# Kernel tuning notes

Hardware: AMD Instinct MI355X
Metric: run time of the kernel (lower is better)

The kernel has to match this reference:

```python
import jax, jax.numpy as jnp
import numpy as np

P_SIZE = 128   # proto_size
HID = 768      # hidden_size
BATCH = 32
NREL = 16
RATIO = 0.5    # proto_emb_ratio


def setup_inputs() -> dict:
    key = jax.random.key(0)
    k1, k2, k3, k4 = jax.random.split(key, 4)
    return {
        "instance_embedding": jax.random.normal(k1, (BATCH, HID), jnp.float32),
        # small scale keeps sigmoid(p_h @ M_r @ p_t) away from hard saturation
        "relation_embedding": jax.random.normal(k2, (NREL, HID, HID), jnp.float32) * 0.02,
        "rel_label_ids": jax.random.randint(k3, (BATCH, NREL, P_SIZE), 0, P_SIZE + 1, dtype=jnp.int32),
        "labels": jnp.arange(BATCH, dtype=jnp.int32),  # distinct -> torch.unique is exact with static shapes
        "prototypes": jax.random.normal(k4, (P_SIZE, HID), jnp.float32),  # nn.Embedding weight
    }


def reference(instance_embedding, relation_embedding, rel_label_ids, labels, prototypes):
    P, H = prototypes.shape
    B, R, _ = rel_label_ids.shape

    # torch.unique(labels, return_inverse=True): sorted uniques + inverse map.
    labels_unique = jnp.sort(labels)                      # [K] (K == B, labels distinct)
    inv = jnp.argsort(jnp.argsort(labels))                # index_list (rank of each label)
    # original code: index = index_list[k] -> rel rows permuted by inverse map
    rel_k = rel_label_ids[inv]                            # [K,R,P]

    total_nonzero = jnp.sum(rel_label_ids) > 0
    batch_mask = (jnp.sum(rel_k, axis=(1, 2)) > 0)[:, None, None]   # skip if sum(rel[index])==0
    row_mask = (jnp.sum(rel_k, axis=2) > 0)[:, :, None]             # skip if sum(rel[index][i])==0
    m = (rel_k != P) & batch_mask & row_mask & total_nonzero        # [K,R,P] active entries
    mf = m.astype(prototypes.dtype)

    P0 = prototypes                                       # get_proto_embedding(): never updated inside loop
    heads = jnp.minimum(rel_k, P - 1)                     # safe gather (masked where == P)
    Ph = P0[heads]                                        # [K,R,P,H]  (largest intermediate)
    pt = P0[labels_unique]                                # [K,H]

    # sim[k,i,j] = sigmoid(P0[head] @ M_r[i] @ P0[label_k])
    v = jnp.einsum('rhg,kg->krh', relation_embedding, pt)           # [K,R,H]
    sim = jax.nn.sigmoid(jnp.einsum('krph,krh->krp', Ph, v))        # [K,R,P]

    # logits_ol init: zeros, then logits_ol[:][:][:][0] = 1.0 sets the k==0 slab to 1.0
    base = jnp.zeros((B, R, P, 2), prototypes.dtype).at[0].set(1.0)
    l1 = jnp.where(m, sim, base[..., 1])
    l0 = jnp.where(m, 1.0 - sim, base[..., 0])
    logits_ol = jnp.stack([l0, l1], axis=-1).reshape(-1, 2)         # [K*R*P, 2]
    labels_ol = m.astype(jnp.int32).reshape(-1)                     # [K*R*P]

    # proto propagation: mean over active (i,j) of P0[head] @ M_r[i]
    w = jnp.einsum('krp,krph->krh', mf, Ph)                         # [K,R,H]
    prop = jnp.einsum('krh,rhg->kg', w, relation_embedding)         # [K,H]
    n = jnp.sum(mf, axis=(1, 2))                                    # num_prop per k
    prop = prop / jnp.maximum(n, 1.0)[:, None]
    old_rows = prototypes[labels_unique]
    new_rows = RATIO * old_rows + (1.0 - RATIO) * prop
    rows = jnp.where((n > 0)[:, None], new_rows, old_rows)
    proto_embedding = prototypes.at[labels_unique].set(rows)        # scatter update (distinct rows)

    # CrossEntropyLoss (mean); 0 when all rel ids are zero (labels_ol would be None)
    logp = jax.nn.log_softmax(logits_ol, axis=-1)
    ce = -jnp.mean(jnp.take_along_axis(logp, labels_ol[:, None], axis=1))
    loss_ol = jnp.where(total_nonzero, ce, 0.0)

    # logits = -||proto - instance||^2 pairwise: [B, P]
    diff = instance_embedding[:, None, :] - proto_embedding[None, :, :]
    logits = -jnp.sum(diff * diff, axis=2)

    return logits, loss_ol, proto_embedding
```

## Files before the change

kernel.cpp:

```cpp
#include <hip/hip_runtime.h>
#include <hip/hip_bf16.h>
#include <math.h>

#define K_B 32
#define NRELD 16
#define PSZ 128
#define HID 768

using bf16x8 = __attribute__((ext_vector_type(8))) short;
using f32x4  = __attribute__((ext_vector_type(4))) float;

__device__ __forceinline__ unsigned int f2bf(float x) {
    unsigned int u = __float_as_uint(x);
    return (u + 0x7fffu + ((u >> 16) & 1u)) >> 16;
}
__device__ __forceinline__ float bf2f(unsigned short b) {
    return __uint_as_float(((unsigned int)b) << 16);
}

__global__ __launch_bounds__(192) void k_prep(
        const int* __restrict__ labels, const int* __restrict__ relIds,
        const float* __restrict__ P0,
        unsigned short* __restrict__ S_bf, unsigned short* __restrict__ P0_bf,
        unsigned short* __restrict__ P0T_bf, unsigned short* __restrict__ pt_bf,
        int* __restrict__ rowflag, int* __restrict__ cntRow,
        int* __restrict__ rowOwner_g)
{
    int bid = blockIdx.x, t = threadIdx.x;
    int k = bid >> 4, r = bid & 15;
    __shared__ int lab[32], rankS[32], luS[32], ownS[128];
    __shared__ int hist[128], redS[128];
    if (t < 32) lab[t] = labels[t];
    if (t < 128) { hist[t] = 0; ownS[t] = -1; }
    __syncthreads();
    if (t < 32) { int rk = 0; for (int j = 0; j < 32; ++j) rk += (lab[j] < lab[t]); rankS[t] = rk; }
    __syncthreads();
    if (t < 32) luS[rankS[t]] = lab[t];
    __syncthreads();
    if (t < 32) ownS[luS[t]] = t;
    __syncthreads();

    int id = 0, isv = 0;
    if (t < 128) {
        id = relIds[((size_t)rankS[k]*NRELD + r)*PSZ + t];
        isv = (id != PSZ);
        if (isv) atomicAdd(&hist[id], 1);
        redS[t] = id + (isv << 20);
    }
    __syncthreads();
    for (int off = 64; off; off >>= 1) {
        if (t < off) redS[t] += redS[t + off];
        __syncthreads();
    }
    int rowsum = redS[0] & 0xFFFFF;
    int cnt    = redS[0] >> 20;
    int rf     = (rowsum > 0);
    if (t < 128)
        S_bf[(size_t)bid*128 + t] = (unsigned short)f2bf(rf ? (float)hist[t] : 0.f);
    if (t == 0) { rowflag[bid] = rf; cntRow[bid] = cnt; }
    if (bid == 0 && t < 128) rowOwner_g[t] = ownS[t];

    if (bid < 128) {
        int p = bid;
        float4 v4 = *(const float4*)&P0[(size_t)p*HID + t*4];
        unsigned int b0 = f2bf(v4.x), b1 = f2bf(v4.y), b2 = f2bf(v4.z), b3 = f2bf(v4.w);
        uint2 d; d.x = b0 | (b1 << 16); d.y = b2 | (b3 << 16);
        *(uint2*)&P0_bf[(size_t)p*HID + t*4] = d;
        P0T_bf[(size_t)(t*4+0)*128 + p] = (unsigned short)b0;
        P0T_bf[(size_t)(t*4+1)*128 + p] = (unsigned short)b1;
        P0T_bf[(size_t)(t*4+2)*128 + p] = (unsigned short)b2;
        P0T_bf[(size_t)(t*4+3)*128 + p] = (unsigned short)b3;
        int kk = ownS[p];
        if (kk >= 0) *(uint2*)&pt_bf[(size_t)kk*HID + t*4] = d;
    }
}

__global__ __launch_bounds__(256) void k_vw(
        const float* __restrict__ rel, const unsigned short* __restrict__ pt_bf,
        const unsigned short* __restrict__ S_bf, const unsigned short* __restrict__ P0T_bf,
        unsigned short* __restrict__ v_bf, unsigned short* __restrict__ w_bf,
        float* __restrict__ prop, float* __restrict__ lossAcc)
{
    __shared__ unsigned short sh[32*768 + 64*128];
    int bid = blockIdx.x, t = threadIdx.x;
    int wave = t >> 6, lane = t & 63;

    if (bid < 192) {
        int r = bid & 15, hs = bid >> 4;
        unsigned short* ptS = sh;
        unsigned short* AS  = sh + 32*768;

        for (int i = t; i < 3072; i += 256) {
            int k = i / 96, c = i % 96;
            uint4 d = *(const uint4*)&pt_bf[(size_t)k*HID + c*8];
            *(uint4*)&ptS[k*768 + (c ^ (k & 7))*8] = d;
        }
        const int gq = (t & 31) * 4;
        const int hr = t >> 5;
        const size_t relbase = ((size_t)r*HID + hs*64) * HID;

        float4 buf[8];
        #pragma unroll
        for (int rr = 0; rr < 8; ++rr)
            buf[rr] = *(const float4*)&rel[relbase + (size_t)(hr + rr*8)*HID + gq];

        f32x4 acc[2] = {{0.f,0.f,0.f,0.f},{0.f,0.f,0.f,0.f}};
        const int arow = wave*16 + (lane & 15);

        for (int gt = 0; gt < 6; ++gt) {
            __syncthreads();
            #pragma unroll
            for (int rr = 0; rr < 8; ++rr) {
                int h_l = hr + rr*8;
                float4 v4 = buf[rr];
                int cs = (gq >> 3) ^ (h_l & 7);
                uint2 d; d.x = f2bf(v4.x) | (f2bf(v4.y) << 16);
                d.y = f2bf(v4.z) | (f2bf(v4.w) << 16);
                *(uint2*)&AS[h_l*128 + cs*8 + (gq & 4)] = d;
            }
            __syncthreads();
            if (gt < 5) {
                int gn = gt*128 + 128;
                #pragma unroll
                for (int rr = 0; rr < 8; ++rr)
                    buf[rr] = *(const float4*)&rel[relbase + (size_t)(hr + rr*8)*HID + gn + gq];
            }
            #pragma unroll
            for (int kk = 0; kk < 4; ++kk) {
                int cA = (kk*4 + (lane >> 4)) ^ (arow & 7);
                bf16x8 a = *(const bf16x8*)&AS[arow*128 + cA*8];
                #pragma unroll
                for (int nf = 0; nf < 2; ++nf) {
                    int k = nf*16 + (lane & 15);
                    int cB = (gt*16 + kk*4 + (lane >> 4)) ^ (k & 7);
                    bf16x8 b = *(const bf16x8*)&ptS[k*768 + cB*8];
                    acc[nf] = __builtin_amdgcn_mfma_f32_16x16x32_bf16(a, b, acc[nf], 0, 0, 0);
                }
            }
        }
        int h_out = hs*64 + wave*16 + (lane >> 4) * 4;
        #pragma unroll
        for (int nf = 0; nf < 2; ++nf) {
            int k = nf*16 + (lane & 15);
            uint2 d; d.x = f2bf(acc[nf][0]) | (f2bf(acc[nf][1]) << 16);
            d.y = f2bf(acc[nf][2]) | (f2bf(acc[nf][3]) << 16);
            *(uint2*)&v_bf[((size_t)k*NRELD + r)*HID + h_out] = d;
        }
    } else {
        int idx = bid - 192;
        int ms = idx / 12, ns = idx % 12;
        unsigned short* AS2 = sh;
        unsigned short* BS2 = sh + 64*128;
        if (t < 64) *(float4*)&prop[idx*256 + t*4] = float4{0.f,0.f,0.f,0.f};
        if (idx == 0 && t == 0) lossAcc[0] = 0.f;

        for (int i = t; i < 1024; i += 256) {
            int row = i >> 4, c = i & 15;
            *(uint4*)&AS2[row*128 + (c ^ (row & 7))*8] =
                *(const uint4*)&S_bf[(size_t)(ms*64 + row)*128 + c*8];
            *(uint4*)&BS2[row*128 + (c ^ (row & 7))*8] =
                *(const uint4*)&P0T_bf[(size_t)(ns*64 + row)*128 + c*8];
        }
        __syncthreads();
        f32x4 acc[4] = {{0.f,0.f,0.f,0.f},{0.f,0.f,0.f,0.f},{0.f,0.f,0.f,0.f},{0.f,0.f,0.f,0.f}};
        int arow = wave*16 + (lane & 15);
        #pragma unroll
        for (int kk = 0; kk < 4; ++kk) {
            int cA = (kk*4 + (lane >> 4)) ^ (arow & 7);
            bf16x8 a = *(const bf16x8*)&AS2[arow*128 + cA*8];
            #pragma unroll
            for (int nf = 0; nf < 4; ++nf) {
                int brow = nf*16 + (lane & 15);
                int cB = (kk*4 + (lane >> 4)) ^ (brow & 7);
                bf16x8 b = *(const bf16x8*)&BS2[brow*128 + cB*8];
                acc[nf] = __builtin_amdgcn_mfma_f32_16x16x32_bf16(a, b, acc[nf], 0, 0, 0);
            }
        }
        int kr0 = ms*64 + wave*16 + (lane >> 4) * 4;
        #pragma unroll
        for (int nf = 0; nf < 4; ++nf) {
            int h = ns*64 + nf*16 + (lane & 15);
            #pragma unroll
            for (int j = 0; j < 4; ++j)
                w_bf[(size_t)(kr0 + j)*HID + h] = (unsigned short)f2bf(acc[nf][j]);
        }
    }
}

__global__ __launch_bounds__(256) void k_prop_mfma(
        const float* __restrict__ rel, const unsigned short* __restrict__ w_bf,
        float* __restrict__ prop)
{
    int r = blockIdx.x, gs = blockIdx.y, t = threadIdx.x;
    int wave = t >> 6, lane = t & 63;
    __shared__ unsigned short WS[32*768];
    __shared__ unsigned short BS[64*128];

    for (int i = t; i < 3072; i += 256) {
        int k = i / 96, c = i % 96;
        uint4 d = *(const uint4*)&w_bf[((size_t)k*NRELD + r)*HID + c*8];
        *(uint4*)&WS[k*768 + (c ^ (k & 7))*8] = d;
    }
    const int gqq = t & 15;
    const int h4  = t >> 4;
    const size_t relb = (size_t)r*HID*HID + (size_t)gs*64;

    float4 buf[8];
    #pragma unroll
    for (int sup = 0; sup < 2; ++sup)
        #pragma unroll
        for (int rr = 0; rr < 4; ++rr)
            buf[sup*4+rr] = *(const float4*)&rel[relb + (size_t)(sup*64 + h4*4 + rr)*HID + gqq*4];

    f32x4 acc[2] = {{0.f,0.f,0.f,0.f},{0.f,0.f,0.f,0.f}};

    for (int ht = 0; ht < 6; ++ht) {
        __syncthreads();
        #pragma unroll
        for (int sup = 0; sup < 2; ++sup) {
            #pragma unroll
            for (int i = 0; i < 4; ++i) {
                int g_l = gqq*4 + i;
                int hloc = sup*64 + h4*4;
                unsigned int p0 = f2bf(((const float*)&buf[sup*4+0])[i]);
                unsigned int p1 = f2bf(((const float*)&buf[sup*4+1])[i]);
                unsigned int p2 = f2bf(((const float*)&buf[sup*4+2])[i]);
                unsigned int p3 = f2bf(((const float*)&buf[sup*4+3])[i]);
                int cs = (hloc >> 3) ^ ((g_l >> 2) & 7);
                uint2 d; d.x = p0 | (p1 << 16); d.y = p2 | (p3 << 16);
                *(uint2*)&BS[g_l*128 + cs*8 + (hloc & 4)] = d;
            }
        }
        __syncthreads();
        if (ht < 5) {
            int hn = ht*128 + 128;
            #pragma unroll
            for (int sup = 0; sup < 2; ++sup)
                #pragma unroll
                for (int rr = 0; rr < 4; ++rr)
                    buf[sup*4+rr] = *(const float4*)&rel[relb + (size_t)(hn + sup*64 + h4*4 + rr)*HID + gqq*4];
        }
        int g_l = wave*16 + (lane & 15);
        #pragma unroll
        for (int kk = 0; kk < 4; ++kk) {
            int cB = (kk*4 + (lane >> 4)) ^ ((g_l >> 2) & 7);
            bf16x8 b = *(const bf16x8*)&BS[g_l*128 + cB*8];
            #pragma unroll
            for (int mf = 0; mf < 2; ++mf) {
                int arow = mf*16 + (lane & 15);
                int cA = (ht*16 + kk*4 + (lane >> 4)) ^ (arow & 7);
                bf16x8 a = *(const bf16x8*)&WS[arow*768 + cA*8];
                acc[mf] = __builtin_amdgcn_mfma_f32_16x16x32_bf16(a, b, acc[mf], 0, 0, 0);
            }
        }
    }
    int gcol = gs*64 + wave*16 + (lane & 15);
    #pragma unroll
    for (int mf = 0; mf < 2; ++mf) {
        int k0 = mf*16 + (lane >> 4) * 4;
        #pragma unroll
        for (int j = 0; j < 4; ++j)
            atomicAdd(&prop[(size_t)(k0 + j)*HID + gcol], acc[mf][j]);
    }
}

__global__ __launch_bounds__(256) void k_zzproto(
        const unsigned short* __restrict__ v_bf, const unsigned short* __restrict__ P0_bf,
        const unsigned short* __restrict__ S_bf, float* __restrict__ lossAcc,
        const float* __restrict__ P0, const float* __restrict__ prop,
        const int* __restrict__ rowflag, const int* __restrict__ cntRow,
        const int* __restrict__ rowOwner_g, float* __restrict__ protoOut)
{
    __shared__ unsigned short sh[16*128 + 128*128];
    __shared__ float red[256];
    __shared__ float nActS[32];
    __shared__ int kS[32];
    int bid = blockIdx.x, t = threadIdx.x;
    int wave = t >> 6, lane = t & 63;

    if (bid < 32) {
        int ms = bid;
        unsigned short* AS  = sh;
        unsigned short* BS2 = sh + 16*128;
        f32x4 acc[2] = {{0.f,0.f,0.f,0.f},{0.f,0.f,0.f,0.f}};
        for (int ht = 0; ht < 6; ++ht) {
            int h0 = ht * 128;
            __syncthreads();
            {
                int row = t >> 4, c = t & 15;
                *(uint4*)&AS[row*128 + (c ^ (row & 7))*8] =
                    *(const uint4*)&v_bf[(size_t)(ms*16 + row)*HID + h0 + c*8];
                #pragma unroll
                for (int q = 0; q < 8; ++q) {
                    int j2 = t + q*256;
                    int prow = j2 >> 4, c2 = j2 & 15;
                    *(uint4*)&BS2[prow*128 + (c2 ^ (prow & 7))*8] =
                        *(const uint4*)&P0_bf[(size_t)prow*HID + h0 + c2*8];
                }
            }
            __syncthreads();
            int arow = lane & 15;
            #pragma unroll
            for (int kk = 0; kk < 4; ++kk) {
                int cA = (kk*4 + (lane >> 4)) ^ (arow & 7);
                bf16x8 a = *(const bf16x8*)&AS[arow*128 + cA*8];
                #pragma unroll
                for (int nf = 0; nf < 2; ++nf) {
                    int brow = wave*32 + nf*16 + (lane & 15);
                    int cB = (kk*4 + (lane >> 4)) ^ (brow & 7);
                    bf16x8 b = *(const bf16x8*)&BS2[brow*128 + cB*8];
                    acc[nf] = __builtin_amdgcn_mfma_f32_16x16x32_bf16(a, b, acc[nf], 0, 0, 0);
                }
            }
        }
        float term = 0.f;
        #pragma unroll
        for (int nf = 0; nf < 2; ++nf) {
            int p = wave*32 + nf*16 + (lane & 15);
            int kr0 = ms*16 + (lane >> 4) * 4;
            #pragma unroll
            for (int j = 0; j < 4; ++j) {
                float S = bf2f(S_bf[(size_t)(kr0 + j)*128 + p]);
                if (S != 0.f) {
                    float z = acc[nf][j];
                    float s = 1.f / (1.f + expf(-z));
                    term += S * (logf(expf(1.f - s) + expf(s)) - s);
                }
            }
        }
        red[t] = term;
        __syncthreads();
        for (int off = 128; off; off >>= 1) {
            if (t < off) red[t] += red[t + off];
            __syncthreads();
        }
        if (t == 0) atomicAdd(lossAcc, red[0]);
    } else {
        int base = (bid - 32) * 32;
        if (t < 32) {
            int p = base + t;
            int k = rowOwner_g[p];
            float n = 0.f;
            if (k >= 0)
                for (int i = 0; i < 16; ++i) {
                    int rr = k*NRELD + i;
                    if (rowflag[rr]) n += (float)cntRow[rr];
                }
            nActS[t] = n; kS[t] = k;
        }
        __syncthreads();
        for (int j = 0; j < 24; ++j) {
            int flat = t + 256*j;
            int pl = flat / 192, c = flat % 192;
            int p = base + pl;
            float4 old = *(const float4*)&P0[(size_t)p*HID + c*4];
            float4 o = old;
            int k = kS[pl]; float n = nActS[pl];
            if (k >= 0 && n > 0.f) {
                float4 pr = *(const float4*)&prop[(size_t)k*HID + c*4];
                float invn = 0.5f / n;
                o.x = 0.5f*old.x + pr.x*invn;
                o.y = 0.5f*old.y + pr.y*invn;
                o.z = 0.5f*old.z + pr.z*invn;
                o.w = 0.5f*old.w + pr.w*invn;
            }
            *(float4*)&protoOut[(size_t)p*HID + c*4] = o;
        }
    }
}

__global__ __launch_bounds__(128) void k_logits(const float* __restrict__ inst,
        const float* __restrict__ protoOut, const float* __restrict__ lossAcc,
        const int* __restrict__ rowflag, const int* __restrict__ cntRow,
        float* __restrict__ outLogits, float* __restrict__ outLoss)
{
    int b = blockIdx.x, t = threadIdx.x;
    __shared__ float iS[768];
    __shared__ float ls[128];
    __shared__ int ts[128];
    for (int q = 0; q < 6; ++q) iS[t + 128*q] = inst[(size_t)b*HID + t + 128*q];
    __syncthreads();
    const float4* pr = (const float4*)&protoOut[(size_t)t*HID];
    float acc = 0.f;
    for (int q = 0; q < HID/4; ++q) {
        float4 pv = pr[q];
        float dx = iS[q*4+0] - pv.x, dy = iS[q*4+1] - pv.y;
        float dz = iS[q*4+2] - pv.z, dw = iS[q*4+3] - pv.w;
        acc += dx*dx + dy*dy + dz*dz + dw*dw;
    }
    outLogits[b*PSZ + t] = -acc;
    if (b == 0) {
        float s = 0.f; int tot = 0;
        #pragma unroll
        for (int q = 0; q < 4; ++q) {
            int rr = t + 128*q;
            int rf = rowflag[rr];
            tot |= rf;
            if (rf) s += (float)cntRow[rr];
        }
        ls[t] = s; ts[t] = tot;
        __syncthreads();
        for (int off = 64; off; off >>= 1) {
            if (t < off) { ls[t] += ls[t + off]; ts[t] |= ts[t + off]; }
            __syncthreads();
        }
        if (t == 0)
            outLoss[0] = ts[0]
                ? (lossAcc[0] + (65536.f - ls[0]) * 0.6931471805599453f) * (1.f/65536.f)
                : 0.f;
    }
}

extern "C" void kernel_launch(void* const* d_in, const int* in_sizes, int n_in,
                              void* d_out, int out_size, void* d_ws, size_t ws_size,
                              hipStream_t stream)
{
    const float* inst  = (const float*)d_in[0];
    const float* rel   = (const float*)d_in[1];
    const int* relIds  = (const int*)d_in[2];
    const int* labels  = (const int*)d_in[3];
    const float* P0    = (const float*)d_in[4];
    float* out = (float*)d_out;
    float* outLogits = out;
    float* outLoss   = out + 4096;
    float* outProto  = out + 4097;

    char* ws = (char*)d_ws;
    unsigned short* v_bf    = (unsigned short*)(ws + 0);
    unsigned short* w_bf    = (unsigned short*)(ws + 786432);
    unsigned short* S_bf    = (unsigned short*)(ws + 1572864);
    unsigned short* P0_bf   = (unsigned short*)(ws + 1703936);
    unsigned short* P0T_bf  = (unsigned short*)(ws + 1900544);
    unsigned short* pt_bf   = (unsigned short*)(ws + 2097152);
    float* prop    = (float*)(ws + 2146304);
    float* lossAcc = (float*)(ws + 2244608);
    int*   rowflag = (int*)(ws + 2244736);
    int*   cntRow  = (int*)(ws + 2246784);
    int*   rowOwner= (int*)(ws + 2248832);

    k_prep<<<512, 192, 0, stream>>>(labels, relIds, P0, S_bf, P0_bf, P0T_bf,
                                    pt_bf, rowflag, cntRow, rowOwner);
    k_vw<<<288, 256, 0, stream>>>(rel, pt_bf, S_bf, P0T_bf, v_bf, w_bf,
                                  prop, lossAcc);
    k_prop_mfma<<<dim3(16,12), 256, 0, stream>>>(rel, w_bf, prop);
    k_zzproto<<<36, 256, 0, stream>>>(v_bf, P0_bf, S_bf, lossAcc, P0, prop,
                                      rowflag, cntRow, rowOwner, outProto);
    k_logits<<<32, 128, 0, stream>>>(inst, outProto, lossAcc, rowflag, cntRow,
                                     outLogits, outLoss);
}
```

Before: 136.5 us.

## Fuse five-kernel pipeline into one cooperative megakernel with grid syncs

Replaces the five sequential kernel launches with a single cooperative kernel of 288 blocks that runs each stage as a phase separated by grid.sync(). Prep, v/w GEMMs, propagation plus loss, and the proto update plus logits reuse the existing block decompositions, with the zzproto and logits work redistributed across the phases. The aim is to remove per-launch overhead and inter-kernel gaps. In exchange it depends on cooperative launch support and full co-residency, needs enough shared memory per block, and pays for grid-wide barriers. It falls back to the original launches if the cooperative launch fails.

```diff
diff --git a/kernel.cpp b/kernel.cpp
--- a/kernel.cpp
+++ b/kernel.cpp
@@ -1,6 +1,9 @@
 #include <hip/hip_runtime.h>
+#include <hip/hip_cooperative_groups.h>
 #include <hip/hip_bf16.h>
 #include <math.h>
+
+namespace cg = cooperative_groups;
 
 #define K_B 32
 #define NRELD 16
@@ -16,6 +19,372 @@
 }
 __device__ __forceinline__ float bf2f(unsigned short b) {
     return __uint_as_float(((unsigned int)b) << 16);
+}
+
+struct MegaParams {
+    const float* inst; const float* rel; const int* relIds;
+    const int* labels; const float* P0;
+    unsigned short *S_bf, *P0_bf, *P0T_bf, *pt_bf, *v_bf, *w_bf;
+    float *prop, *lossAcc;
+    int *rowflag, *cntRow;
+    float *outLogits, *outLoss, *outProto;
+};
+
+__global__ __launch_bounds__(256) void k_mega(MegaParams P)
+{
+    cg::grid_group grid = cg::this_grid();
+    __shared__ unsigned short sh[32*768 + 64*128];
+    __shared__ int lab[32], rankS[32], luS[32], ownS[128];
+    __shared__ int hist[2][128], redS[256];
+    __shared__ float redF[256];
+    __shared__ float nActS[16];
+    __shared__ int kS2[16];
+    const int bid = blockIdx.x, t = threadIdx.x;
+    const int wave = t >> 6, lane = t & 63;
+
+    if (t < 32) lab[t] = P.labels[t];
+    if (t < 128) ownS[t] = -1;
+    hist[t >> 7][t & 127] = 0;
+    __syncthreads();
+    if (t < 32) { int rk = 0; for (int j = 0; j < 32; ++j) rk += (lab[j] < lab[t]); rankS[t] = rk; }
+    __syncthreads();
+    if (t < 32) luS[rankS[t]] = lab[t];
+    __syncthreads();
+    if (t < 32) ownS[luS[t]] = t;
+    __syncthreads();
+
+    if (bid < 256) {
+        int half = t >> 7, j = t & 127;
+        int row = bid*2 + half;
+        int k = row >> 4, r = row & 15;
+        int id = P.relIds[((size_t)rankS[k]*NRELD + r)*PSZ + j];
+        int isv = (id != PSZ);
+        if (isv) atomicAdd(&hist[half][id], 1);
+        redS[t] = id + (isv << 20);
+        __syncthreads();
+        for (int off = 64; off; off >>= 1) {
+            if (j < off) redS[t] += redS[t + off];
+            __syncthreads();
+        }
+        int rowsum = redS[half << 7] & 0xFFFFF;
+        int cnt    = redS[half << 7] >> 20;
+        int rf     = (rowsum > 0);
+        P.S_bf[(size_t)row*128 + j] = (unsigned short)f2bf(rf ? (float)hist[half][j] : 0.f);
+        if (j == 0) { P.rowflag[row] = rf; P.cntRow[row] = cnt; }
+    } else {
+        int pb = (bid - 256) * 4;
+        if (t < 192) {
+            for (int rr = 0; rr < 4; ++rr) {
+                int p = pb + rr;
+                float4 v4 = *(const float4*)&P.P0[(size_t)p*HID + t*4];
+                unsigned int b0 = f2bf(v4.x), b1 = f2bf(v4.y), b2 = f2bf(v4.z), b3 = f2bf(v4.w);
+                uint2 d; d.x = b0 | (b1 << 16); d.y = b2 | (b3 << 16);
+                *(uint2*)&P.P0_bf[(size_t)p*HID + t*4] = d;
+                P.P0T_bf[(size_t)(t*4+0)*128 + p] = (unsigned short)b0;
+                P.P0T_bf[(size_t)(t*4+1)*128 + p] = (unsigned short)b1;
+                P.P0T_bf[(size_t)(t*4+2)*128 + p] = (unsigned short)b2;
+                P.P0T_bf[(size_t)(t*4+3)*128 + p] = (unsigned short)b3;
+                int kk = ownS[p];
+                if (kk >= 0) *(uint2*)&P.pt_bf[(size_t)kk*HID + t*4] = d;
+            }
+        }
+    }
+    grid.sync();
+
+    if (bid < 192) {
+        int r = bid & 15, hs = bid >> 4;
+        unsigned short* ptS = sh;
+        unsigned short* AS  = sh + 32*768;
+        for (int i = t; i < 3072; i += 256) {
+            int k = i / 96, c = i % 96;
+            uint4 d = *(const uint4*)&P.pt_bf[(size_t)k*HID + c*8];
+            *(uint4*)&ptS[k*768 + (c ^ (k & 7))*8] = d;
+        }
+        const int gq = (t & 31) * 4;
+        const int hr = t >> 5;
+        const size_t relbase = ((size_t)r*HID + hs*64) * HID;
+        float4 buf[8];
+        #pragma unroll
+        for (int rr = 0; rr < 8; ++rr)
+            buf[rr] = *(const float4*)&P.rel[relbase + (size_t)(hr + rr*8)*HID + gq];
+        f32x4 acc[2] = {{0.f,0.f,0.f,0.f},{0.f,0.f,0.f,0.f}};
+        const int arow = wave*16 + (lane & 15);
+        for (int gt = 0; gt < 6; ++gt) {
+            __syncthreads();
+            #pragma unroll
+            for (int rr = 0; rr < 8; ++rr) {
+                int h_l = hr + rr*8;
+                float4 v4 = buf[rr];
+                int cs = (gq >> 3) ^ (h_l & 7);
+                uint2 d; d.x = f2bf(v4.x) | (f2bf(v4.y) << 16);
+                d.y = f2bf(v4.z) | (f2bf(v4.w) << 16);
+                *(uint2*)&AS[h_l*128 + cs*8 + (gq & 4)] = d;
+            }
+            __syncthreads();
+            if (gt < 5) {
+                int gn = gt*128 + 128;
+                #pragma unroll
+                for (int rr = 0; rr < 8; ++rr)
+                    buf[rr] = *(const float4*)&P.rel[relbase + (size_t)(hr + rr*8)*HID + gn + gq];
+            }
+            #pragma unroll
+            for (int kk = 0; kk < 4; ++kk) {
+                int cA = (kk*4 + (lane >> 4)) ^ (arow & 7);
+                bf16x8 a = *(const bf16x8*)&AS[arow*128 + cA*8];
+                #pragma unroll
+                for (int nf = 0; nf < 2; ++nf) {
+                    int k = nf*16 + (lane & 15);
+                    int cB = (gt*16 + kk*4 + (lane >> 4)) ^ (k & 7);
+                    bf16x8 b = *(const bf16x8*)&ptS[k*768 + cB*8];
+                    acc[nf] = __builtin_amdgcn_mfma_f32_16x16x32_bf16(a, b, acc[nf], 0, 0, 0);
+                }
+            }
+        }
+        int h_out = hs*64 + wave*16 + (lane >> 4) * 4;
+        #pragma unroll
+        for (int nf = 0; nf < 2; ++nf) {
+            int k = nf*16 + (lane & 15);
+            uint2 d; d.x = f2bf(acc[nf][0]) | (f2bf(acc[nf][1]) << 16);
+            d.y = f2bf(acc[nf][2]) | (f2bf(acc[nf][3]) << 16);
+            *(uint2*)&P.v_bf[((size_t)k*NRELD + r)*HID + h_out] = d;
+        }
+    } else {
+        int idx = bid - 192;
+        int ms = idx / 12, ns = idx % 12;
+        unsigned short* AS2 = sh;
+        unsigned short* BS2 = sh + 64*128;
+        if (t < 64) *(float4*)&P.prop[idx*256 + t*4] = float4{0.f,0.f,0.f,0.f};
+        if (idx == 0 && t == 0) P.lossAcc[0] = 0.f;
+        for (int i = t; i < 1024; i += 256) {
+            int row = i >> 4, c = i & 15;
+            *(uint4*)&AS2[row*128 + (c ^ (row & 7))*8] =
+                *(const uint4*)&P.S_bf[(size_t)(ms*64 + row)*128 + c*8];
+            *(uint4*)&BS2[row*128 + (c ^ (row & 7))*8] =
+                *(const uint4*)&P.P0T_bf[(size_t)(ns*64 + row)*128 + c*8];
+        }
+        __syncthreads();
+        f32x4 acc[4] = {{0.f,0.f,0.f,0.f},{0.f,0.f,0.f,0.f},{0.f,0.f,0.f,0.f},{0.f,0.f,0.f,0.f}};
+        int arow = wave*16 + (lane & 15);
+        #pragma unroll
+        for (int kk = 0; kk < 4; ++kk) {
+            int cA = (kk*4 + (lane >> 4)) ^ (arow & 7);
+            bf16x8 a = *(const bf16x8*)&AS2[arow*128 + cA*8];
+            #pragma unroll
+            for (int nf = 0; nf < 4; ++nf) {
+                int brow = nf*16 + (lane & 15);
+                int cB = (kk*4 + (lane >> 4)) ^ (brow & 7);
+                bf16x8 b = *(const bf16x8*)&BS2[brow*128 + cB*8];
+                acc[nf] = __builtin_amdgcn_mfma_f32_16x16x32_bf16(a, b, acc[nf], 0, 0, 0);
+            }
+        }
+        int kr0 = ms*64 + wave*16 + (lane >> 4) * 4;
+        #pragma unroll
+        for (int nf = 0; nf < 4; ++nf) {
+            int h = ns*64 + nf*16 + (lane & 15);
+            #pragma unroll
+            for (int j = 0; j < 4; ++j)
+                P.w_bf[(size_t)(kr0 + j)*HID + h] = (unsigned short)f2bf(acc[nf][j]);
+        }
+    }
+    grid.sync();
+
+    if (bid < 192) {
+        int r = bid & 15, gs = bid >> 4;
+        unsigned short* WS = sh;
+        unsigned short* BS = sh + 32*768;
+        for (int i = t; i < 3072; i += 256) {
+            int k = i / 96, c = i % 96;
+            uint4 d = *(const uint4*)&P.w_bf[((size_t)k*NRELD + r)*HID + c*8];
+            *(uint4*)&WS[k*768 + (c ^ (k & 7))*8] = d;
+        }
+        const int gqq = t & 15;
+        const int h4  = t >> 4;
+        const size_t relb = (size_t)r*HID*HID + (size_t)gs*64;
+        float4 buf[8];
+        #pragma unroll
+        for (int sup = 0; sup < 2; ++sup)
+            #pragma unroll
+            for (int rr = 0; rr < 4; ++rr)
+                buf[sup*4+rr] = *(const float4*)&P.rel[relb + (size_t)(sup*64 + h4*4 + rr)*HID + gqq*4];
+        f32x4 acc[2] = {{0.f,0.f,0.f,0.f},{0.f,0.f,0.f,0.f}};
+        for (int ht = 0; ht < 6; ++ht) {
+            __syncthreads();
+            #pragma unroll
+            for (int sup = 0; sup < 2; ++sup) {
+                #pragma unroll
+                for (int i = 0; i < 4; ++i) {
+                    int g_l = gqq*4 + i;
+                    int hloc = sup*64 + h4*4;
+                    unsigned int p0 = f2bf(((const float*)&buf[sup*4+0])[i]);
+                    unsigned int p1 = f2bf(((const float*)&buf[sup*4+1])[i]);
+                    unsigned int p2 = f2bf(((const float*)&buf[sup*4+2])[i]);
+                    unsigned int p3 = f2bf(((const float*)&buf[sup*4+3])[i]);
+                    int cs = (hloc >> 3) ^ ((g_l >> 2) & 7);
+                    uint2 d; d.x = p0 | (p1 << 16); d.y = p2 | (p3 << 16);
+                    *(uint2*)&BS[g_l*128 + cs*8 + (hloc & 4)] = d;
+                }
+            }
+            __syncthreads();
+            if (ht < 5) {
+                int hn = ht*128 + 128;
+                #pragma unroll
+                for (int sup = 0; sup < 2; ++sup)
+                    #pragma unroll
+                    for (int rr = 0; rr < 4; ++rr)
+                        buf[sup*4+rr] = *(const float4*)&P.rel[relb + (size_t)(hn + sup*64 + h4*4 + rr)*HID + gqq*4];
+            }
+            int g_l = wave*16 + (lane & 15);
+            #pragma unroll
+            for (int kk = 0; kk < 4; ++kk) {
+                int cB = (kk*4 + (lane >> 4)) ^ ((g_l >> 2) & 7);
+                bf16x8 b = *(const bf16x8*)&BS[g_l*128 + cB*8];
+                #pragma unroll
+                for (int mf = 0; mf < 2; ++mf) {
+                    int arow = mf*16 + (lane & 15);
+                    int cA = (ht*16 + kk*4 + (lane >> 4)) ^ (arow & 7);
+                    bf16x8 a = *(const bf16x8*)&WS[arow*768 + cA*8];
+                    acc[mf] = __builtin_amdgcn_mfma_f32_16x16x32_bf16(a, b, acc[mf], 0, 0, 0);
+                }
+            }
+        }
+        int gcol = gs*64 + wave*16 + (lane & 15);
+        #pragma unroll
+        for (int mf = 0; mf < 2; ++mf) {
+            int k0 = mf*16 + (lane >> 4) * 4;
+            #pragma unroll
+            for (int j = 0; j < 4; ++j)
+                atomicAdd(&P.prop[(size_t)(k0 + j)*HID + gcol], acc[mf][j]);
+        }
+    } else if (bid < 224) {
+        int ms = bid - 192;
+        unsigned short* AS  = sh;
+        unsigned short* BS2 = sh + 16*128;
+        f32x4 acc[2] = {{0.f,0.f,0.f,0.f},{0.f,0.f,0.f,0.f}};
+        for (int ht = 0; ht < 6; ++ht) {
+            int h0 = ht * 128;
+            __syncthreads();
+            {
+                int row = t >> 4, c = t & 15;
+                *(uint4*)&AS[row*128 + (c ^ (row & 7))*8] =
+                    *(const uint4*)&P.v_bf[(size_t)(ms*16 + row)*HID + h0 + c*8];
+                #pragma unroll
+                for (int q = 0; q < 8; ++q) {
+                    int j2 = t + q*256;
+                    int prow = j2 >> 4, c2 = j2 & 15;
+                    *(uint4*)&BS2[prow*128 + (c2 ^ (prow & 7))*8] =
+                        *(const uint4*)&P.P0_bf[(size_t)prow*HID + h0 + c2*8];
+                }
+            }
+            __syncthreads();
+            int arow = lane & 15;
+            #pragma unroll
+            for (int kk = 0; kk < 4; ++kk) {
+                int cA = (kk*4 + (lane >> 4)) ^ (arow & 7);
+                bf16x8 a = *(const bf16x8*)&AS[arow*128 + cA*8];
+                #pragma unroll
+                for (int nf = 0; nf < 2; ++nf) {
+                    int brow = wave*32 + nf*16 + (lane & 15);
+                    int cB = (kk*4 + (lane >> 4)) ^ (brow & 7);
+                    bf16x8 b = *(const bf16x8*)&BS2[brow*128 + cB*8];
+                    acc[nf] = __builtin_amdgcn_mfma_f32_16x16x32_bf16(a, b, acc[nf], 0, 0, 0);
+                }
+            }
+        }
+        float term = 0.f;
+        #pragma unroll
+        for (int nf = 0; nf < 2; ++nf) {
+            int p = wave*32 + nf*16 + (lane & 15);
+            int kr0 = ms*16 + (lane >> 4) * 4;
+            #pragma unroll
+            for (int j = 0; j < 4; ++j) {
+                float S = bf2f(P.S_bf[(size_t)(kr0 + j)*128 + p]);
+                if (S != 0.f) {
+                    float z = acc[nf][j];
+                    float s = 1.f / (1.f + expf(-z));
+                    term += S * (logf(expf(1.f - s) + expf(s)) - s);
+                }
+            }
+        }
+        redF[t] = term;
+        __syncthreads();
+        for (int off = 128; off; off >>= 1) {
+            if (t < off) redF[t] += redF[t + off];
+            __syncthreads();
+        }
+        if (t == 0) atomicAdd(P.lossAcc, redF[0]);
+    }
+    grid.sync();
+
+    if (bid < 8) {
+        float* protoS = (float*)sh;
+        const int PSTR = 772;
+        if (t < 16) {
+            int p = bid*16 + t;
+            int k = ownS[p];
+            float n = 0.f;
+            if (k >= 0)
+                for (int i = 0; i < 16; ++i) {
+                    int rr2 = k*NRELD + i;
+                    if (P.rowflag[rr2]) n += (float)P.cntRow[rr2];
+                }
+            nActS[t] = n; kS2[t] = k;
+        }
+        __syncthreads();
+        for (int it = t; it < 16*192; it += 256) {
+            int pl = it / 192, c = it % 192;
+            int p = bid*16 + pl;
+            float4 old = *(const float4*)&P.P0[(size_t)p*HID + c*4];
+            float4 o = old;
+            int k = kS2[pl]; float n = nActS[pl];
+            if (k >= 0 && n > 0.f) {
+                float4 pr = *(const float4*)&P.prop[(size_t)k*HID + c*4];
+                float invn = 0.5f / n;
+                o.x = 0.5f*old.x + pr.x*invn;
+                o.y = 0.5f*old.y + pr.y*invn;
+                o.z = 0.5f*old.z + pr.z*invn;
+                o.w = 0.5f*old.w + pr.w*invn;
+            }
+            *(float4*)&P.outProto[(size_t)p*HID + c*4] = o;
+            protoS[pl*PSTR + c*4+0] = o.x;
+            protoS[pl*PSTR + c*4+1] = o.y;
+            protoS[pl*PSTR + c*4+2] = o.z;
+            protoS[pl*PSTR + c*4+3] = o.w;
+        }
+        __syncthreads();
+        int b = t & 31, p2 = (t >> 5) * 2;
+        const float4* ir = (const float4*)&P.inst[(size_t)b*HID];
+        float a0 = 0.f, a1 = 0.f;
+        for (int q = 0; q < HID/4; ++q) {
+            float4 iv = ir[q];
+            float4 pv0 = *(const float4*)&protoS[p2*PSTR + q*4];
+            float4 pv1 = *(const float4*)&protoS[(p2+1)*PSTR + q*4];
+            float dx = iv.x - pv0.x, dy = iv.y - pv0.y, dz = iv.z - pv0.z, dw = iv.w - pv0.w;
+            a0 += dx*dx + dy*dy + dz*dz + dw*dw;
+            dx = iv.x - pv1.x; dy = iv.y - pv1.y; dz = iv.z - pv1.z; dw = iv.w - pv1.w;
+            a1 += dx*dx + dy*dy + dz*dz + dw*dw;
+        }
+        P.outLogits[b*PSZ + bid*16 + p2]     = -a0;
+        P.outLogits[b*PSZ + bid*16 + p2 + 1] = -a1;
+    } else if (bid == 8) {
+        float s = 0.f; int tot = 0;
+        #pragma unroll
+        for (int q = 0; q < 2; ++q) {
+            int rr2 = t + 256*q;
+            int rf = P.rowflag[rr2];
+            tot |= rf;
+            if (rf) s += (float)P.cntRow[rr2];
+        }
+        redF[t] = s; redS[t] = tot;
+        __syncthreads();
+        for (int off = 128; off; off >>= 1) {
+            if (t < off) { redF[t] += redF[t + off]; redS[t] |= redS[t + off]; }
+            __syncthreads();
+        }
+        if (t == 0)
+            P.outLoss[0] = redS[0]
+                ? (P.lossAcc[0] + (65536.f - redF[0]) * 0.6931471805599453f) * (1.f/65536.f)
+                : 0.f;
+    }
 }
 
 __global__ __launch_bounds__(192) void k_prep(
@@ -39,7 +408,6 @@
     __syncthreads();
     if (t < 32) ownS[luS[t]] = t;
     __syncthreads();
-
     int id = 0, isv = 0;
     if (t < 128) {
         id = relIds[((size_t)rankS[k]*NRELD + r)*PSZ + t];
@@ -59,7 +427,6 @@
         S_bf[(size_t)bid*128 + t] = (unsigned short)f2bf(rf ? (float)hist[t] : 0.f);
     if (t == 0) { rowflag[bid] = rf; cntRow[bid] = cnt; }
     if (bid == 0 && t < 128) rowOwner_g[t] = ownS[t];
-
     if (bid < 128) {
         int p = bid;
         float4 v4 = *(const float4*)&P0[(size_t)p*HID + t*4];
@@ -84,12 +451,10 @@
     __shared__ unsigned short sh[32*768 + 64*128];
     int bid = blockIdx.x, t = threadIdx.x;
     int wave = t >> 6, lane = t & 63;
-
     if (bid < 192) {
         int r = bid & 15, hs = bid >> 4;
         unsigned short* ptS = sh;
         unsigned short* AS  = sh + 32*768;
-
         for (int i = t; i < 3072; i += 256) {
             int k = i / 96, c = i % 96;
             uint4 d = *(const uint4*)&pt_bf[(size_t)k*HID + c*8];
@@ -98,15 +463,12 @@
         const int gq = (t & 31) * 4;
         const int hr = t >> 5;
         const size_t relbase = ((size_t)r*HID + hs*64) * HID;
-
         float4 buf[8];
         #pragma unroll
         for (int rr = 0; rr < 8; ++rr)
             buf[rr] = *(const float4*)&rel[relbase + (size_t)(hr + rr*8)*HID + gq];
-
         f32x4 acc[2] = {{0.f,0.f,0.f,0.f},{0.f,0.f,0.f,0.f}};
         const int arow = wave*16 + (lane & 15);
-
         for (int gt = 0; gt < 6; ++gt) {
             __syncthreads();
             #pragma unroll
@@ -153,7 +515,6 @@
         unsigned short* BS2 = sh + 64*128;
         if (t < 64) *(float4*)&prop[idx*256 + t*4] = float4{0.f,0.f,0.f,0.f};
         if (idx == 0 && t == 0) lossAcc[0] = 0.f;
-
         for (int i = t; i < 1024; i += 256) {
             int row = i >> 4, c = i & 15;
             *(uint4*)&AS2[row*128 + (c ^ (row & 7))*8] =
@@ -195,7 +556,6 @@
     int wave = t >> 6, lane = t & 63;
     __shared__ unsigned short WS[32*768];
     __shared__ unsigned short BS[64*128];
-
     for (int i = t; i < 3072; i += 256) {
         int k = i / 96, c = i % 96;
         uint4 d = *(const uint4*)&w_bf[((size_t)k*NRELD + r)*HID + c*8];
@@ -204,16 +564,13 @@
     const int gqq = t & 15;
     const int h4  = t >> 4;
     const size_t relb = (size_t)r*HID*HID + (size_t)gs*64;
-
     float4 buf[8];
     #pragma unroll
     for (int sup = 0; sup < 2; ++sup)
         #pragma unroll
         for (int rr = 0; rr < 4; ++rr)
             buf[sup*4+rr] = *(const float4*)&rel[relb + (size_t)(sup*64 + h4*4 + rr)*HID + gqq*4];
-
     f32x4 acc[2] = {{0.f,0.f,0.f,0.f},{0.f,0.f,0.f,0.f}};
-
     for (int ht = 0; ht < 6; ++ht) {
         __syncthreads();
         #pragma unroll
@@ -277,7 +634,6 @@
     __shared__ int kS[32];
     int bid = blockIdx.x, t = threadIdx.x;
     int wave = t >> 6, lane = t & 63;
-
     if (bid < 32) {
         int ms = bid;
         unsigned short* AS  = sh;
@@ -438,13 +794,26 @@
     int*   cntRow  = (int*)(ws + 2246784);
     int*   rowOwner= (int*)(ws + 2248832);
 
-    k_prep<<<512, 192, 0, stream>>>(labels, relIds, P0, S_bf, P0_bf, P0T_bf,
-                                    pt_bf, rowflag, cntRow, rowOwner);
-    k_vw<<<288, 256, 0, stream>>>(rel, pt_bf, S_bf, P0T_bf, v_bf, w_bf,
-                                  prop, lossAcc);
-    k_prop_mfma<<<dim3(16,12), 256, 0, stream>>>(rel, w_bf, prop);
-    k_zzproto<<<36, 256, 0, stream>>>(v_bf, P0_bf, S_bf, lossAcc, P0, prop,
-                                      rowflag, cntRow, rowOwner, outProto);
-    k_logits<<<32, 128, 0, stream>>>(inst, outProto, lossAcc, rowflag, cntRow,
-                                     outLogits, outLoss);
+    MegaParams Pm;
+    Pm.inst = inst; Pm.rel = rel; Pm.relIds = relIds; Pm.labels = labels; Pm.P0 = P0;
+    Pm.S_bf = S_bf; Pm.P0_bf = P0_bf; Pm.P0T_bf = P0T_bf; Pm.pt_bf = pt_bf;
+    Pm.v_bf = v_bf; Pm.w_bf = w_bf; Pm.prop = prop; Pm.lossAcc = lossAcc;
+    Pm.rowflag = rowflag; Pm.cntRow = cntRow;
+    Pm.outLogits = outLogits; Pm.outLoss = outLoss; Pm.outProto = outProto;
+
+    void* args[] = { &Pm };
+    hipError_t err = hipLaunchCooperativeKernel((const void*)k_mega,
+                                                dim3(288), dim3(256),
+                                                args, 0, stream);
+    if (err != hipSuccess) {
+        k_prep<<<512, 192, 0, stream>>>(labels, relIds, P0, S_bf, P0_bf, P0T_bf,
+                                        pt_bf, rowflag, cntRow, rowOwner);
+        k_vw<<<288, 256, 0, stream>>>(rel, pt_bf, S_bf, P0T_bf, v_bf, w_bf,
+                                      prop, lossAcc);
+        k_prop_mfma<<<dim3(16,12), 256, 0, stream>>>(rel, w_bf, prop);
+        k_zzproto<<<36, 256, 0, stream>>>(v_bf, P0_bf, S_bf, lossAcc, P0, prop,
+                                          rowflag, cntRow, rowOwner, outProto);
+        k_logits<<<32, 128, 0, stream>>>(inst, outProto, lossAcc, rowflag, cntRow,
+                                         outLogits, outLoss);
+    }
 }
```

Result: slower. 250.3 us (+83.4%).
